# Optimization experiments

Hardware: AMD Instinct MI355X
Metric: run time of the kernel (lower is better)

Reference implementation:

```python
import jax, jax.numpy as jnp
import numpy as np

T, B, D, H = 512, 64, 1024, 1024


def setup_inputs() -> dict:
    key = jax.random.key(0)
    ks = jax.random.split(key, 6)
    s_in = 0.02  # small init so tanh/sigmoid don't saturate
    return {
        "x": jax.random.normal(ks[0], (T, B, D), jnp.float32),
        "Wih": jax.random.normal(ks[1], (D, 4 * H), jnp.float32) * s_in,
        "Whh": jax.random.normal(ks[2], (H, 4 * H), jnp.float32) * s_in,
        "b": jnp.zeros((4 * H,), jnp.float32),
        "Wih_r": jax.random.normal(ks[3], (D, 4 * H), jnp.float32) * s_in,
        "Whh_r": jax.random.normal(ks[4], (H, 4 * H), jnp.float32) * s_in,
        "b_r": jnp.zeros((4 * H,), jnp.float32),
    }


def _lstm_scan(x, Wih, Whh, b):
    """Run an LSTM over time-major x [T,B,D]; returns (hs [T,B,H], h_T, c_T)."""
    Bsz = x.shape[1]
    h0 = jnp.zeros((Bsz, H), x.dtype)
    c0 = jnp.zeros((Bsz, H), x.dtype)

    # Precompute input projections for all timesteps in one big GEMM.
    xg = jnp.einsum("tbd,dg->tbg", x, Wih) + b  # [T,B,4H]

    def step(carry, xg_t):
        h, c = carry
        gates = xg_t + h @ Whh  # [B,4H]
        i, f, g, o = jnp.split(gates, 4, axis=-1)
        c_next = jax.nn.sigmoid(f) * c + jax.nn.sigmoid(i) * jnp.tanh(g)
        h_next = jax.nn.sigmoid(o) * jnp.tanh(c_next)
        return (h_next, c_next), h_next

    (hT, cT), hs = jax.lax.scan(step, (h0, c0), xg)
    return hs, hT, cT


def reference(x, Wih, Whh, b, Wih_r, Whh_r, b_r):
    # forward direction
    hs_f, hT, cT = _lstm_scan(x, Wih, Whh, b)
    # backward direction: flip time, run, flip outputs back
    hs_b, _, _ = _lstm_scan(x[::-1], Wih_r, Whh_r, b_r)
    output = jnp.concatenate([hs_f, hs_b[::-1]], axis=-1)  # [T,B,2H]
    # original returns (output, h_n) where h_n is the forward cell's final (h, c)
    return output, hT, cT
```

## Files before the change

### kernel.cpp

```cpp
#include <hip/hip_runtime.h>
#include <hip/hip_bf16.h>


#define TS    512
#define BATCH 64
#define DDIM  1024
#define HDIM  1024
#define KD    2048
#define GD    4096
#define OUT_HS ((size_t)TS * BATCH * 2 * HDIM)
#define HT_OFF OUT_HS
#define CT_OFF (OUT_HS + (size_t)BATCH * HDIM)

#define WP_BYTES   ((size_t)2 * GD * KD * 2)
#define XBF_BYTES  ((size_t)TS * BATCH * DDIM * 2)
#define HS_BYTES   ((size_t)2 * 2 * BATCH * HDIM * 2)
#define BAR_BYTES  ((size_t)4096)
#define WS_A_TOTAL (WP_BYTES + XBF_BYTES + HS_BYTES + BAR_BYTES)
#define WS_B_TOTAL (WP_BYTES + HS_BYTES + BAR_BYTES)

typedef __attribute__((ext_vector_type(8))) short frag8;
typedef __attribute__((ext_vector_type(4))) float f32x4;
typedef unsigned long long u64;

__device__ __forceinline__ ushort f2b(float f) {
  union { float f; unsigned u; } v; v.f = f;
  unsigned r = v.u + 0x7FFFu + ((v.u >> 16) & 1u);
  return (ushort)(r >> 16);
}
__device__ __forceinline__ float sigf(float x) { return 1.0f / (1.0f + __expf(-x)); }
__device__ __forceinline__ float tanh_fast(float x) {
  x = fminf(15.0f, fmaxf(-15.0f, x));
  float e = __expf(2.0f * x);
  return (e - 1.0f) / (e + 1.0f);
}


__global__ void xconv(const float* __restrict__ x, ushort* __restrict__ o) {
  size_t i = ((size_t)blockIdx.x * 256 + threadIdx.x) * 8;
  float4 a = *(const float4*)(x + i);
  float4 b = *(const float4*)(x + i + 4);
  union { ushort s[8]; uint4 v; } r;
  r.s[0] = f2b(a.x); r.s[1] = f2b(a.y); r.s[2] = f2b(a.z); r.s[3] = f2b(a.w);
  r.s[4] = f2b(b.x); r.s[5] = f2b(b.y); r.s[6] = f2b(b.z); r.s[7] = f2b(b.w);
  *(uint4*)(o + i) = r.v;
}

__global__ void wpackk(const float* __restrict__ Wih,  const float* __restrict__ Whh,
                       const float* __restrict__ WihR, const float* __restrict__ WhhR,
                       ushort* __restrict__ wp) {
  __shared__ ushort tile[32][36];
  int bid = blockIdx.x;
  int kt  = bid & 63;
  int pt  = (bid >> 6) & 127;
  int dir = bid >> 13;
  const float* Wi = dir ? WihR : Wih;
  const float* Wh = dir ? WhhR : Whh;
  int t  = threadIdx.x;
  int kl = t >> 3;
  int g  = (t >> 1) & 3;
  int q  = t & 1;
  int k  = kt * 32 + kl;
  const float* srow = (k < 1024) ? (Wi + (size_t)k * GD) : (Wh + (size_t)(k - 1024) * GD);
  float4 v = *(const float4*)(srow + g * 1024 + pt * 8 + q * 4);
  int pl = g * 8 + q * 4;
  tile[kl][pl + 0] = f2b(v.x); tile[kl][pl + 1] = f2b(v.y);
  tile[kl][pl + 2] = f2b(v.z); tile[kl][pl + 3] = f2b(v.w);
  __syncthreads();
  int po = t >> 3;
  int kc = t & 7;
  ushort* dst = wp + ((size_t)dir * GD + pt * 32 + po) * KD + kt * 32 + kc * 4;
  ushort4 ov;
  ov.x = tile[kc * 4 + 0][po]; ov.y = tile[kc * 4 + 1][po];
  ov.z = tile[kc * 4 + 2][po]; ov.w = tile[kc * 4 + 3][po];
  *(ushort4*)dst = ov;
}

#define MFMA(a, b, c) __builtin_amdgcn_mfma_f32_16x16x32_bf16((a), (b), (c), 0, 0, 0)
#define ALOADU64(p) __hip_atomic_load((p), __ATOMIC_RELAXED, __HIP_MEMORY_SCOPE_AGENT)
#define SB() __builtin_amdgcn_sched_barrier(0)

template <int MODEA>
__global__ __launch_bounds__(256, 1)
void lstm_scan(const ushort* __restrict__ xbf, const float* __restrict__ xf,
               const ushort* __restrict__ wpack,
               const float* __restrict__ bfwd, const float* __restrict__ bbwd,
               ushort* hstate, float* __restrict__ out, unsigned* bar) {
  __shared__ ushort wlds[32 * KD];

  const int tid  = threadIdx.x;
  const int lane = tid & 63;
  const int wv   = tid >> 6;
  const int wg   = blockIdx.x;
  const int dir  = wg >> 7;
  const int wq   = wg & 127;
  unsigned* grpflags = bar + (dir * 4 + wv) * 128;

  {
    const ushort* src = wpack + ((size_t)dir * GD + wq * 32) * KD;
#pragma unroll
    for (int it = 0; it < 32; ++it) {
      int m  = it * 256 + tid;
      int p  = m >> 8;
      int kc = m & 255;
      uint4 v = *(const uint4*)(src + (size_t)p * KD + kc * 8);
      int off = p * 4096 + ((kc * 16) ^ ((p & 7) << 4));
      *(uint4*)((char*)wlds + off) = v;
    }
  }
  __syncthreads();

  const int lm   = lane & 15;
  const int jj   = lane & 7;
  const int kb   = (lane >> 4) * 8;
  const int kb2  = kb * 2;
  const int arow = wv * 16 + lm;
  const int hcol = wq * 8 + jj;
  const int sw   = jj << 4;
  const int b0base = lm * 4096;
  const int b1base = (16 + lm) * 4096;

  const float* bsrc = dir ? bbwd : bfwd;
  const float bias0 = bsrc[(lm >> 3) * HDIM + hcol];
  const float bias1 = bsrc[(2 + (lm >> 3)) * HDIM + hcol];

  float creg[4] = {0.f, 0.f, 0.f, 0.f};
  float hvv[4];
  f32x4 a0a, a0b, a1a, a1b;

  auto compute_x = [&](int tt) {
    const int tsrc = dir ? (TS - 1 - tt) : tt;
    a0a = (f32x4){0.f,0.f,0.f,0.f}; a0b = (f32x4){0.f,0.f,0.f,0.f};
    a1a = (f32x4){0.f,0.f,0.f,0.f}; a1b = (f32x4){0.f,0.f,0.f,0.f};
    if (MODEA) {
      const ushort* xs = xbf + ((size_t)tsrc * BATCH + arow) * DDIM + kb;
#pragma unroll 8
      for (int kk = 0; kk < 32; kk += 2) {
        frag8 a  = *(const frag8*)(xs + kk * 32);
        frag8 a2 = *(const frag8*)(xs + (kk + 1) * 32);
        int ko  = (kk * 64 + kb2) ^ sw;
        int ko2 = ((kk + 1) * 64 + kb2) ^ sw;
        frag8 b0  = *(const frag8*)((const char*)wlds + (b0base + ko));
        frag8 b1  = *(const frag8*)((const char*)wlds + (b1base + ko));
        frag8 b02 = *(const frag8*)((const char*)wlds + (b0base + ko2));
        frag8 b12 = *(const frag8*)((const char*)wlds + (b1base + ko2));
        a0a = MFMA(a, b0, a0a);  a1a = MFMA(a, b1, a1a);
        a0b = MFMA(a2, b02, a0b); a1b = MFMA(a2, b12, a1b);
      }
    } else {
      const float* xs = xf + ((size_t)tsrc * BATCH + arow) * DDIM + kb;
#pragma unroll 4
      for (int kk = 0; kk < 32; ++kk) {
        float4 f0 = *(const float4*)(xs + kk * 32);
        float4 f1 = *(const float4*)(xs + kk * 32 + 4);
        union { ushort s[8]; frag8 fr; } ua;
        ua.s[0] = f2b(f0.x); ua.s[1] = f2b(f0.y); ua.s[2] = f2b(f0.z); ua.s[3] = f2b(f0.w);
        ua.s[4] = f2b(f1.x); ua.s[5] = f2b(f1.y); ua.s[6] = f2b(f1.z); ua.s[7] = f2b(f1.w);
        int ko = (kk * 64 + kb2) ^ sw;
        frag8 b0 = *(const frag8*)((const char*)wlds + (b0base + ko));
        frag8 b1 = *(const frag8*)((const char*)wlds + (b1base + ko));
        if (kk & 1) { a0b = MFMA(ua.fr, b0, a0b); a1b = MFMA(ua.fr, b1, a1b); }
        else        { a0a = MFMA(ua.fr, b0, a0a); a1a = MFMA(ua.fr, b1, a1a); }
      }
    }
  };

  auto h_part = [&](int t) {
    const ushort* hsrd = hstate + (((size_t)(t & 1) * 2 + dir) * BATCH + arow) * HDIM + kb;
    frag8 hf[32];
#pragma unroll
    for (int kk = 0; kk < 32; ++kk)
      asm volatile("global_load_dwordx4 %0, %1, off offset:%2 sc1"
                   : "=v"(hf[kk]) : "v"(hsrd), "i"(kk * 64) : "memory");
    asm volatile("s_waitcnt vmcnt(0)" ::: "memory");
    SB();
#pragma unroll
    for (int kk = 0; kk < 32; kk += 2) {
      int ko  = (2048 + kk * 64 + kb2) ^ sw;
      int ko2 = (2048 + (kk + 1) * 64 + kb2) ^ sw;
      frag8 b0  = *(const frag8*)((const char*)wlds + (b0base + ko));
      frag8 b1  = *(const frag8*)((const char*)wlds + (b1base + ko));
      frag8 b02 = *(const frag8*)((const char*)wlds + (b0base + ko2));
      frag8 b12 = *(const frag8*)((const char*)wlds + (b1base + ko2));
      a0a = MFMA(hf[kk], b0, a0a);      a1a = MFMA(hf[kk], b1, a1a);
      a0b = MFMA(hf[kk + 1], b02, a0b); a1b = MFMA(hf[kk + 1], b12, a1b);
    }
  };

  compute_x(0);

  for (int t = 0; t < TS; ++t) {
    if (t > 0) h_part(t);

    const int tsrc = dir ? (TS - 1 - t) : t;
    f32x4 acc0 = a0a + a0b;
    f32x4 acc1 = a1a + a1b;

    ushort* hnext = hstate + ((size_t)(((t + 1) & 1) * 2 + dir) * BATCH) * HDIM;
    const size_t obase = ((size_t)tsrc * BATCH) * (2 * HDIM) + (size_t)dir * HDIM + hcol;
    const bool last = (t == TS - 1);
    const bool last_f = (dir == 0) && last;

#pragma unroll
    for (int i = 0; i < 4; ++i) {
      float g0 = acc0[i] + bias0;
      float g1 = acc1[i] + bias1;
      float q0 = __shfl_xor(g0, 8);
      float q1 = __shfl_xor(g1, 8);
      if ((lane & 8) == 0) {
        float cn = sigf(q0) * creg[i] + sigf(g0) * tanh_fast(g1);
        creg[i] = cn;
        hvv[i] = sigf(q1) * tanh_fast(cn);
      }
    }

    if (!last) {
#pragma unroll
      for (int i = 0; i < 4; ++i) {
        if ((lane & 8) == 0) {
          int brow = wv * 16 + (lane >> 4) * 4 + i;
          __hip_atomic_store(hnext + (size_t)brow * HDIM + hcol, f2b(hvv[i]),
                             __ATOMIC_RELAXED, __HIP_MEMORY_SCOPE_AGENT);
        }
      }
    }
    SB();
#pragma unroll
    for (int i = 0; i < 4; ++i) {
      if ((lane & 8) == 0) {
        int brow = wv * 16 + (lane >> 4) * 4 + i;
        __builtin_nontemporal_store(hvv[i], out + obase + (size_t)brow * (2 * HDIM));
      }
    }
    if (last_f) {
#pragma unroll
      for (int i = 0; i < 4; ++i) {
        if ((lane & 8) == 0) {
          int brow = wv * 16 + (lane >> 4) * 4 + i;
          __builtin_nontemporal_store(hvv[i], out + HT_OFF + (size_t)brow * HDIM + hcol);
          __builtin_nontemporal_store(creg[i], out + CT_OFF + (size_t)brow * HDIM + hcol);
        }
      }
    }

    if (last) break;

    asm volatile("s_waitcnt vmcnt(4)" ::: "memory");
    if (lane == 0)
      __hip_atomic_store(grpflags + wq, (unsigned)(t + 1),
                         __ATOMIC_RELAXED, __HIP_MEMORY_SCOPE_AGENT);

    compute_x(t + 1);

    {
      const unsigned want = (unsigned)(t + 1);
      const u64* f2 = (const u64*)grpflags + lane;
      for (;;) {
        u64 v = ALOADU64(f2);
        if ((unsigned)v >= want && (unsigned)(v >> 32) >= want) break;
        __builtin_amdgcn_s_sleep(1);
      }
    }
    __atomic_signal_fence(__ATOMIC_SEQ_CST);
    asm volatile("" ::: "memory");
  }
}

extern "C" void kernel_launch(void* const* d_in, const int* in_sizes, int n_in,
                              void* d_out, int out_size, void* d_ws, size_t ws_size,
                              hipStream_t stream) {
  const float* x    = (const float*)d_in[0];
  const float* Wih  = (const float*)d_in[1];
  const float* Whh  = (const float*)d_in[2];
  const float* b    = (const float*)d_in[3];
  const float* WihR = (const float*)d_in[4];
  const float* WhhR = (const float*)d_in[5];
  const float* bR   = (const float*)d_in[6];
  float* out = (float*)d_out;
  char* ws = (char*)d_ws;

  if (ws_size < WS_B_TOTAL) return;
  const bool modeA = (ws_size >= WS_A_TOTAL);

  ushort* wp  = (ushort*)(ws);
  ushort* xbf = (ushort*)(ws + WP_BYTES);
  size_t hs_off = modeA ? (WP_BYTES + XBF_BYTES) : WP_BYTES;
  ushort* hs = (ushort*)(ws + hs_off);
  unsigned* bar = (unsigned*)(ws + hs_off + HS_BYTES);

  hipMemsetAsync(ws + hs_off + HS_BYTES, 0, BAR_BYTES, stream);

  wpackk<<<dim3(16384), dim3(256), 0, stream>>>(Wih, Whh, WihR, WhhR, wp);

  if (modeA) {
    xconv<<<dim3(16384), dim3(256), 0, stream>>>(x, xbf);
    lstm_scan<1><<<dim3(256), dim3(256), 0, stream>>>(xbf, x, wp, b, bR, hs, out, bar);
  } else {
    lstm_scan<0><<<dim3(256), dim3(256), 0, stream>>>(nullptr, x, wp, b, bR, hs, out, bar);
  }
}
```

Before: 4.379 ms.

## Split K across waves with register-resident weights and LDS partial-sum reduction

In the bf16-x path, each wave now owns a quarter of the K dimension for all 64 batch rows. It keeps its slice of the input and recurrent weights in registers instead of re-reading them from LDS every step. Partial accumulators are exchanged through LDS using per-wave flags and reduced before the gate math. The h-state buffer goes from double to triple buffering, and each wave's grid-wide poll now waits on flags published by all wave groups. The goal is to remove repeated LDS weight traffic and spread the h dependency across waves. The cost is extra LDS round-trips, more register pressure, and an intra-block spin on every step.

Result: slower. 5.516 ms (+26.0%).

```diff
diff --git a/kernel.cpp b/kernel.cpp
--- a/kernel.cpp
+++ b/kernel.cpp
@@ -14,7 +14,7 @@
 
 #define WP_BYTES   ((size_t)2 * GD * KD * 2)
 #define XBF_BYTES  ((size_t)TS * BATCH * DDIM * 2)
-#define HS_BYTES   ((size_t)2 * 2 * BATCH * HDIM * 2)
+#define HS_BYTES   ((size_t)3 * 2 * BATCH * HDIM * 2)
 #define BAR_BYTES  ((size_t)4096)
 #define WS_A_TOTAL (WP_BYTES + XBF_BYTES + HS_BYTES + BAR_BYTES)
 #define WS_B_TOTAL (WP_BYTES + HS_BYTES + BAR_BYTES)
@@ -87,6 +87,7 @@
                const float* __restrict__ bfwd, const float* __restrict__ bbwd,
                ushort* hstate, float* __restrict__ out, unsigned* bar) {
   __shared__ ushort wlds[32 * KD];
+  __shared__ unsigned pflag[64];
 
   const int tid  = threadIdx.x;
   const int lane = tid & 63;
@@ -94,7 +95,7 @@
   const int wg   = blockIdx.x;
   const int dir  = wg >> 7;
   const int wq   = wg & 127;
-  unsigned* grpflags = bar + (dir * 4 + wv) * 128;
+  unsigned* pubflag = bar + (dir * 4 + wv) * 128 + wq;
 
   {
     const ushort* src = wpack + ((size_t)dir * GD + wq * 32) * KD;
@@ -108,13 +109,13 @@
       *(uint4*)((char*)wlds + off) = v;
     }
   }
+  if (tid < 64) pflag[tid] = 0;
   __syncthreads();
 
   const int lm   = lane & 15;
   const int jj   = lane & 7;
-  const int kb   = (lane >> 4) * 8;
-  const int kb2  = kb * 2;
-  const int arow = wv * 16 + lm;
+  const int kg   = lane >> 4;
+  const int kb2  = kg * 16;
   const int hcol = wq * 8 + jj;
   const int sw   = jj << 4;
   const int b0base = lm * 4096;
@@ -126,28 +127,185 @@
 
   float creg[4] = {0.f, 0.f, 0.f, 0.f};
   float hvv[4];
-  f32x4 a0a, a0b, a1a, a1b;
-
-  auto compute_x = [&](int tt) {
-    const int tsrc = dir ? (TS - 1 - tt) : tt;
-    a0a = (f32x4){0.f,0.f,0.f,0.f}; a0b = (f32x4){0.f,0.f,0.f,0.f};
-    a1a = (f32x4){0.f,0.f,0.f,0.f}; a1b = (f32x4){0.f,0.f,0.f,0.f};
-    if (MODEA) {
-      const ushort* xs = xbf + ((size_t)tsrc * BATCH + arow) * DDIM + kb;
-#pragma unroll 8
-      for (int kk = 0; kk < 32; kk += 2) {
-        frag8 a  = *(const frag8*)(xs + kk * 32);
-        frag8 a2 = *(const frag8*)(xs + (kk + 1) * 32);
-        int ko  = (kk * 64 + kb2) ^ sw;
-        int ko2 = ((kk + 1) * 64 + kb2) ^ sw;
-        frag8 b0  = *(const frag8*)((const char*)wlds + (b0base + ko));
-        frag8 b1  = *(const frag8*)((const char*)wlds + (b1base + ko));
-        frag8 b02 = *(const frag8*)((const char*)wlds + (b0base + ko2));
-        frag8 b12 = *(const frag8*)((const char*)wlds + (b1base + ko2));
-        a0a = MFMA(a, b0, a0a);  a1a = MFMA(a, b1, a1a);
-        a0b = MFMA(a2, b02, a0b); a1b = MFMA(a2, b12, a1b);
-      }
-    } else {
+
+  if (MODEA) {
+    frag8 Bx0[8], Bx1[8], Bh0[8], Bh1[8];
+#pragma unroll
+    for (int ks = 0; ks < 8; ++ks) {
+      int k0 = (((wv * 8 + ks) * 64 + kb2) ^ sw);
+      int k1 = ((2048 + (wv * 8 + ks) * 64 + kb2) ^ sw);
+      Bx0[ks] = *(const frag8*)((const char*)wlds + b0base + k0);
+      Bx1[ks] = *(const frag8*)((const char*)wlds + b1base + k0);
+      Bh0[ks] = *(const frag8*)((const char*)wlds + b0base + k1);
+      Bh1[ks] = *(const frag8*)((const char*)wlds + b1base + k1);
+    }
+    __syncthreads();
+    f32x4* pb = (f32x4*)wlds;
+
+    f32x4 pacc0[4], pacc1[4];
+
+    auto compute_x = [&](int tt) {
+      const int tsrc = dir ? (TS - 1 - tt) : tt;
+      const ushort* xs = xbf + (size_t)tsrc * BATCH * DDIM + wv * 256 + kg * 8;
+#pragma unroll
+      for (int rt = 0; rt < 4; ++rt) {
+        pacc0[rt] = (f32x4){0.f,0.f,0.f,0.f};
+        pacc1[rt] = (f32x4){0.f,0.f,0.f,0.f};
+      }
+#pragma unroll
+      for (int rt = 0; rt < 4; ++rt) {
+        const ushort* p = xs + (size_t)(rt * 16 + lm) * DDIM;
+        frag8 f[8];
+#pragma unroll
+        for (int ks = 0; ks < 8; ++ks) f[ks] = *(const frag8*)(p + ks * 32);
+#pragma unroll
+        for (int ks = 0; ks < 8; ++ks) {
+          pacc0[rt] = MFMA(f[ks], Bx0[ks], pacc0[rt]);
+          pacc1[rt] = MFMA(f[ks], Bx1[ks], pacc1[rt]);
+        }
+      }
+    };
+
+    auto h_part = [&](int t) {
+      const ushort* hb = hstate + (((size_t)(t % 3) * 2 + dir) * BATCH + lm) * HDIM
+                         + wv * 256 + kg * 8;
+      frag8 hf[32];
+#pragma unroll
+      for (int rt = 0; rt < 4; ++rt) {
+        const ushort* pr = hb + (size_t)(rt * 16) * HDIM;
+#pragma unroll
+        for (int ks = 0; ks < 8; ++ks)
+          asm volatile("global_load_dwordx4 %0, %1, off offset:%2 sc1"
+                       : "=v"(hf[rt * 8 + ks]) : "v"(pr), "i"(ks * 64) : "memory");
+      }
+      asm volatile("s_waitcnt vmcnt(0)" ::: "memory");
+      SB();
+#pragma unroll
+      for (int rt = 0; rt < 4; ++rt)
+#pragma unroll
+        for (int ks = 0; ks < 8; ++ks) {
+          pacc0[rt] = MFMA(hf[rt * 8 + ks], Bh0[ks], pacc0[rt]);
+          pacc1[rt] = MFMA(hf[rt * 8 + ks], Bh1[ks], pacc1[rt]);
+        }
+    };
+
+    auto gpoll = [&](int gen) {
+      const unsigned want = (unsigned)gen;
+      const int wvp = lane >> 4;
+      const u64* f2 = (const u64*)(bar + (dir * 4 + wvp) * 128 + wv * 32) + (lane & 15);
+      for (;;) {
+        u64 v = ALOADU64(f2);
+        if ((unsigned)v >= want && (unsigned)(v >> 32) >= want) break;
+        __builtin_amdgcn_s_sleep(1);
+      }
+      __atomic_signal_fence(__ATOMIC_SEQ_CST);
+      asm volatile("" ::: "memory");
+    };
+
+    compute_x(0);
+
+    for (int t = 0; t < TS; ++t) {
+      if (t > 0) h_part(t);
+
+      const int par = t & 1;
+      {
+        int wbase = ((par * 4 + wv) * 4) * 2 * 64;
+#pragma unroll
+        for (int rt = 0; rt < 4; ++rt) {
+          pb[wbase + (rt * 2 + 0) * 64 + lane] = pacc0[rt];
+          pb[wbase + (rt * 2 + 1) * 64 + lane] = pacc1[rt];
+        }
+        asm volatile("s_waitcnt lgkmcnt(0)" ::: "memory");
+        SB();
+        if (lane == 0)
+          __hip_atomic_store(&pflag[wv * 16], (unsigned)(t + 1),
+                             __ATOMIC_RELAXED, __HIP_MEMORY_SCOPE_WORKGROUP);
+        for (;;) {
+          unsigned m0 = __hip_atomic_load(&pflag[0],  __ATOMIC_RELAXED, __HIP_MEMORY_SCOPE_WORKGROUP);
+          unsigned m1 = __hip_atomic_load(&pflag[16], __ATOMIC_RELAXED, __HIP_MEMORY_SCOPE_WORKGROUP);
+          unsigned m2 = __hip_atomic_load(&pflag[32], __ATOMIC_RELAXED, __HIP_MEMORY_SCOPE_WORKGROUP);
+          unsigned m3 = __hip_atomic_load(&pflag[48], __ATOMIC_RELAXED, __HIP_MEMORY_SCOPE_WORKGROUP);
+          if (m0 > (unsigned)t && m1 > (unsigned)t && m2 > (unsigned)t && m3 > (unsigned)t) break;
+          __builtin_amdgcn_s_sleep(1);
+        }
+        SB();
+        asm volatile("" ::: "memory");
+      }
+      f32x4 acc0 = (f32x4){0.f,0.f,0.f,0.f};
+      f32x4 acc1 = (f32x4){0.f,0.f,0.f,0.f};
+#pragma unroll
+      for (int w = 0; w < 4; ++w) {
+        int rbase = ((par * 4 + w) * 4 + wv) * 2 * 64;
+        acc0 += pb[rbase + 0 * 64 + lane];
+        acc1 += pb[rbase + 1 * 64 + lane];
+      }
+
+      const int tsrc = dir ? (TS - 1 - t) : t;
+      ushort* hnext = hstate + ((size_t)(((t + 1) % 3) * 2 + dir) * BATCH) * HDIM;
+      const size_t obase = ((size_t)tsrc * BATCH) * (2 * HDIM) + (size_t)dir * HDIM + hcol;
+      const bool last = (t == TS - 1);
+      const bool last_f = (dir == 0) && last;
+
+#pragma unroll
+      for (int i = 0; i < 4; ++i) {
+        float g0 = acc0[i] + bias0;
+        float g1 = acc1[i] + bias1;
+        float q0 = __shfl_xor(g0, 8);
+        float q1 = __shfl_xor(g1, 8);
+        if ((lane & 8) == 0) {
+          float cn = sigf(q0) * creg[i] + sigf(g0) * tanh_fast(g1);
+          creg[i] = cn;
+          hvv[i] = sigf(q1) * tanh_fast(cn);
+        }
+      }
+      if (!last) {
+#pragma unroll
+        for (int i = 0; i < 4; ++i) {
+          if ((lane & 8) == 0) {
+            int brow = wv * 16 + (lane >> 4) * 4 + i;
+            __hip_atomic_store(hnext + (size_t)brow * HDIM + hcol, f2b(hvv[i]),
+                               __ATOMIC_RELAXED, __HIP_MEMORY_SCOPE_AGENT);
+          }
+        }
+      }
+      SB();
+#pragma unroll
+      for (int i = 0; i < 4; ++i) {
+        if ((lane & 8) == 0) {
+          int brow = wv * 16 + (lane >> 4) * 4 + i;
+          __builtin_nontemporal_store(hvv[i], out + obase + (size_t)brow * (2 * HDIM));
+        }
+      }
+      if (last_f) {
+#pragma unroll
+        for (int i = 0; i < 4; ++i) {
+          if ((lane & 8) == 0) {
+            int brow = wv * 16 + (lane >> 4) * 4 + i;
+            __builtin_nontemporal_store(hvv[i], out + HT_OFF + (size_t)brow * HDIM + hcol);
+            __builtin_nontemporal_store(creg[i], out + CT_OFF + (size_t)brow * HDIM + hcol);
+          }
+        }
+      }
+
+      if (last) break;
+
+      asm volatile("s_waitcnt vmcnt(4)" ::: "memory");
+      if (lane == 0)
+        __hip_atomic_store(pubflag, (unsigned)(t + 1),
+                           __ATOMIC_RELAXED, __HIP_MEMORY_SCOPE_AGENT);
+
+      compute_x(t + 1);
+      gpoll(t + 1);
+    }
+  } else {
+    const int kb = kg * 8;
+    const int arow = wv * 16 + lm;
+    unsigned* grpflags = bar + (dir * 4 + wv) * 128;
+    f32x4 a0a, a0b, a1a, a1b;
+    auto compute_x_old = [&](int tt) {
+      const int tsrc = dir ? (TS - 1 - tt) : tt;
+      a0a = (f32x4){0.f,0.f,0.f,0.f}; a0b = (f32x4){0.f,0.f,0.f,0.f};
+      a1a = (f32x4){0.f,0.f,0.f,0.f}; a1b = (f32x4){0.f,0.f,0.f,0.f};
       const float* xs = xf + ((size_t)tsrc * BATCH + arow) * DDIM + kb;
 #pragma unroll 4
       for (int kk = 0; kk < 32; ++kk) {
@@ -156,113 +314,82 @@
         union { ushort s[8]; frag8 fr; } ua;
         ua.s[0] = f2b(f0.x); ua.s[1] = f2b(f0.y); ua.s[2] = f2b(f0.z); ua.s[3] = f2b(f0.w);
         ua.s[4] = f2b(f1.x); ua.s[5] = f2b(f1.y); ua.s[6] = f2b(f1.z); ua.s[7] = f2b(f1.w);
-        int ko = (kk * 64 + kb2) ^ sw;
+        int ko = (kk * 64 + kb * 2) ^ sw;
         frag8 b0 = *(const frag8*)((const char*)wlds + (b0base + ko));
         frag8 b1 = *(const frag8*)((const char*)wlds + (b1base + ko));
         if (kk & 1) { a0b = MFMA(ua.fr, b0, a0b); a1b = MFMA(ua.fr, b1, a1b); }
         else        { a0a = MFMA(ua.fr, b0, a0a); a1a = MFMA(ua.fr, b1, a1a); }
       }
+    };
+    auto h_part_old = [&](int t) {
+      const ushort* hsrd = hstate + (((size_t)(t % 3) * 2 + dir) * BATCH + arow) * HDIM + kb;
+      frag8 hf[32];
+#pragma unroll
+      for (int kk = 0; kk < 32; ++kk)
+        asm volatile("global_load_dwordx4 %0, %1, off offset:%2 sc1"
+                     : "=v"(hf[kk]) : "v"(hsrd), "i"(kk * 64) : "memory");
+      asm volatile("s_waitcnt vmcnt(0)" ::: "memory");
+      SB();
+#pragma unroll
+      for (int kk = 0; kk < 32; kk += 2) {
+        int ko  = (2048 + kk * 64 + kb * 2) ^ sw;
+        int ko2 = (2048 + (kk + 1) * 64 + kb * 2) ^ sw;
+        frag8 b0  = *(const frag8*)((const char*)wlds + (b0base + ko));
+        frag8 b1  = *(const frag8*)((const char*)wlds + (b1base + ko));
+        frag8 b02 = *(const frag8*)((const char*)wlds + (b0base + ko2));
+        frag8 b12 = *(const frag8*)((const char*)wlds + (b1base + ko2));
+        a0a = MFMA(hf[kk], b0, a0a);      a1a = MFMA(hf[kk], b1, a1a);
+        a0b = MFMA(hf[kk + 1], b02, a0b); a1b = MFMA(hf[kk + 1], b12, a1b);
+      }
+    };
+    compute_x_old(0);
+    for (int t = 0; t < TS; ++t) {
+      if (t > 0) h_part_old(t);
+      const int tsrc = dir ? (TS - 1 - t) : t;
+      f32x4 acc0 = a0a + a0b, acc1 = a1a + a1b;
+      ushort* hnext = hstate + ((size_t)(((t + 1) % 3) * 2 + dir) * BATCH) * HDIM;
+      const size_t obase = ((size_t)tsrc * BATCH) * (2 * HDIM) + (size_t)dir * HDIM + hcol;
+      const bool last = (t == TS - 1);
+      const bool last_f = (dir == 0) && last;
+#pragma unroll
+      for (int i = 0; i < 4; ++i) {
+        float g0 = acc0[i] + bias0;
+        float g1 = acc1[i] + bias1;
+        float q0 = __shfl_xor(g0, 8);
+        float q1 = __shfl_xor(g1, 8);
+        if ((lane & 8) == 0) {
+          float cn = sigf(q0) * creg[i] + sigf(g0) * tanh_fast(g1);
+          creg[i] = cn;
+          float hv = sigf(q1) * tanh_fast(cn);
+          int brow = wv * 16 + (lane >> 4) * 4 + i;
+          out[obase + (size_t)brow * (2 * HDIM)] = hv;
+          if (!last)
+            __hip_atomic_store(hnext + (size_t)brow * HDIM + hcol, f2b(hv),
+                               __ATOMIC_RELAXED, __HIP_MEMORY_SCOPE_AGENT);
+          if (last_f) {
+            out[HT_OFF + (size_t)brow * HDIM + hcol] = hv;
+            out[CT_OFF + (size_t)brow * HDIM + hcol] = cn;
+          }
+        }
+      }
+      if (last) break;
+      asm volatile("s_waitcnt vmcnt(0)" ::: "memory");
+      if (lane == 0)
+        __hip_atomic_store(grpflags + wq, (unsigned)(t + 1),
+                           __ATOMIC_RELAXED, __HIP_MEMORY_SCOPE_AGENT);
+      compute_x_old(t + 1);
+      {
+        const unsigned want = (unsigned)(t + 1);
+        const u64* f2 = (const u64*)grpflags + lane;
+        for (;;) {
+          u64 v = ALOADU64(f2);
+          if ((unsigned)v >= want && (unsigned)(v >> 32) >= want) break;
+          __builtin_amdgcn_s_sleep(1);
+        }
+      }
+      __atomic_signal_fence(__ATOMIC_SEQ_CST);
+      asm volatile("" ::: "memory");
     }
-  };
-
-  auto h_part = [&](int t) {
-    const ushort* hsrd = hstate + (((size_t)(t & 1) * 2 + dir) * BATCH + arow) * HDIM + kb;
-    frag8 hf[32];
-#pragma unroll
-    for (int kk = 0; kk < 32; ++kk)
-      asm volatile("global_load_dwordx4 %0, %1, off offset:%2 sc1"
-                   : "=v"(hf[kk]) : "v"(hsrd), "i"(kk * 64) : "memory");
-    asm volatile("s_waitcnt vmcnt(0)" ::: "memory");
-    SB();
-#pragma unroll
-    for (int kk = 0; kk < 32; kk += 2) {
-      int ko  = (2048 + kk * 64 + kb2) ^ sw;
-      int ko2 = (2048 + (kk + 1) * 64 + kb2) ^ sw;
-      frag8 b0  = *(const frag8*)((const char*)wlds + (b0base + ko));
-      frag8 b1  = *(const frag8*)((const char*)wlds + (b1base + ko));
-      frag8 b02 = *(const frag8*)((const char*)wlds + (b0base + ko2));
-      frag8 b12 = *(const frag8*)((const char*)wlds + (b1base + ko2));
-      a0a = MFMA(hf[kk], b0, a0a);      a1a = MFMA(hf[kk], b1, a1a);
-      a0b = MFMA(hf[kk + 1], b02, a0b); a1b = MFMA(hf[kk + 1], b12, a1b);
-    }
-  };
-
-  compute_x(0);
-
-  for (int t = 0; t < TS; ++t) {
-    if (t > 0) h_part(t);
-
-    const int tsrc = dir ? (TS - 1 - t) : t;
-    f32x4 acc0 = a0a + a0b;
-    f32x4 acc1 = a1a + a1b;
-
-    ushort* hnext = hstate + ((size_t)(((t + 1) & 1) * 2 + dir) * BATCH) * HDIM;
-    const size_t obase = ((size_t)tsrc * BATCH) * (2 * HDIM) + (size_t)dir * HDIM + hcol;
-    const bool last = (t == TS - 1);
-    const bool last_f = (dir == 0) && last;
-
-#pragma unroll
-    for (int i = 0; i < 4; ++i) {
-      float g0 = acc0[i] + bias0;
-      float g1 = acc1[i] + bias1;
-      float q0 = __shfl_xor(g0, 8);
-      float q1 = __shfl_xor(g1, 8);
-      if ((lane & 8) == 0) {
-        float cn = sigf(q0) * creg[i] + sigf(g0) * tanh_fast(g1);
-        creg[i] = cn;
-        hvv[i] = sigf(q1) * tanh_fast(cn);
-      }
-    }
-
-    if (!last) {
-#pragma unroll
-      for (int i = 0; i < 4; ++i) {
-        if ((lane & 8) == 0) {
-          int brow = wv * 16 + (lane >> 4) * 4 + i;
-          __hip_atomic_store(hnext + (size_t)brow * HDIM + hcol, f2b(hvv[i]),
-                             __ATOMIC_RELAXED, __HIP_MEMORY_SCOPE_AGENT);
-        }
-      }
-    }
-    SB();
-#pragma unroll
-    for (int i = 0; i < 4; ++i) {
-      if ((lane & 8) == 0) {
-        int brow = wv * 16 + (lane >> 4) * 4 + i;
-        __builtin_nontemporal_store(hvv[i], out + obase + (size_t)brow * (2 * HDIM));
-      }
-    }
-    if (last_f) {
-#pragma unroll
-      for (int i = 0; i < 4; ++i) {
-        if ((lane & 8) == 0) {
-          int brow = wv * 16 + (lane >> 4) * 4 + i;
-          __builtin_nontemporal_store(hvv[i], out + HT_OFF + (size_t)brow * HDIM + hcol);
-          __builtin_nontemporal_store(creg[i], out + CT_OFF + (size_t)brow * HDIM + hcol);
-        }
-      }
-    }
-
-    if (last) break;
-
-    asm volatile("s_waitcnt vmcnt(4)" ::: "memory");
-    if (lane == 0)
-      __hip_atomic_store(grpflags + wq, (unsigned)(t + 1),
-                         __ATOMIC_RELAXED, __HIP_MEMORY_SCOPE_AGENT);
-
-    compute_x(t + 1);
-
-    {
-      const unsigned want = (unsigned)(t + 1);
-      const u64* f2 = (const u64*)grpflags + lane;
-      for (;;) {
-        u64 v = ALOADU64(f2);
-        if ((unsigned)v >= want && (unsigned)(v >> 32) >= want) break;
-        __builtin_amdgcn_s_sleep(1);
-      }
-    }
-    __atomic_signal_fence(__ATOMIC_SEQ_CST);
-    asm volatile("" ::: "memory");
   }
 }
 
```

## Split K dimension across two wave groups per block with LDS partial-sum reduction

Applied to the files above, without the earlier changes.

Doubles the block to 512 threads so that each of the four row waves gets a partner wave handling the other half of the K dimension for both the x and h projections. The partner writes its partial accumulators to shared memory and signals through a workgroup-scope LDS flag, and the primary wave adds them before computing the gates. This halves the serial per-wave MFMA and h-load chain on the recurrent critical path. In exchange it adds an intra-block handoff and more waves contending for LDS bandwidth. The fallback mode keeps the old single-wave path and lets the extra waves exit early.

Measured after the change: 4.916 ms. 1.12x slower.

```diff
diff --git a/kernel.cpp b/kernel.cpp
--- a/kernel.cpp
+++ b/kernel.cpp
@@ -81,16 +81,20 @@
 #define SB() __builtin_amdgcn_sched_barrier(0)
 
 template <int MODEA>
-__global__ __launch_bounds__(256, 1)
+__global__ __launch_bounds__(512, 1)
 void lstm_scan(const ushort* __restrict__ xbf, const float* __restrict__ xf,
                const ushort* __restrict__ wpack,
                const float* __restrict__ bfwd, const float* __restrict__ bbwd,
                ushort* hstate, float* __restrict__ out, unsigned* bar) {
   __shared__ ushort wlds[32 * KD];
+  __shared__ f32x4 pbuf[2][4][2][64];
+  __shared__ unsigned hflag[2][4][16];
 
   const int tid  = threadIdx.x;
   const int lane = tid & 63;
-  const int wv   = tid >> 6;
+  const int w8   = tid >> 6;
+  const int wv   = w8 & 3;
+  const int khalf= w8 >> 2;
   const int wg   = blockIdx.x;
   const int dir  = wg >> 7;
   const int wq   = wg & 127;
@@ -99,8 +103,8 @@
   {
     const ushort* src = wpack + ((size_t)dir * GD + wq * 32) * KD;
 #pragma unroll
-    for (int it = 0; it < 32; ++it) {
-      int m  = it * 256 + tid;
+    for (int it = 0; it < 16; ++it) {
+      int m  = it * 512 + tid;
       int p  = m >> 8;
       int kc = m & 255;
       uint4 v = *(const uint4*)(src + (size_t)p * KD + kc * 8);
@@ -108,17 +112,20 @@
       *(uint4*)((char*)wlds + off) = v;
     }
   }
+  if (tid < 128) ((unsigned*)hflag)[tid] = 0;
   __syncthreads();
 
   const int lm   = lane & 15;
   const int jj   = lane & 7;
-  const int kb   = (lane >> 4) * 8;
+  const int kg   = lane >> 4;
+  const int kb   = kg * 8;
   const int kb2  = kb * 2;
   const int arow = wv * 16 + lm;
   const int hcol = wq * 8 + jj;
   const int sw   = jj << 4;
   const int b0base = lm * 4096;
   const int b1base = (16 + lm) * 4096;
+  const int ksb  = khalf * 16;
 
   const float* bsrc = dir ? bbwd : bfwd;
   const float bias0 = bsrc[(lm >> 3) * HDIM + hcol];
@@ -128,18 +135,30 @@
   float hvv[4];
   f32x4 a0a, a0b, a1a, a1b;
 
-  auto compute_x = [&](int tt) {
-    const int tsrc = dir ? (TS - 1 - tt) : tt;
-    a0a = (f32x4){0.f,0.f,0.f,0.f}; a0b = (f32x4){0.f,0.f,0.f,0.f};
-    a1a = (f32x4){0.f,0.f,0.f,0.f}; a1b = (f32x4){0.f,0.f,0.f,0.f};
-    if (MODEA) {
-      const ushort* xs = xbf + ((size_t)tsrc * BATCH + arow) * DDIM + kb;
+  auto poll = [&](int gen) {
+    const unsigned want = (unsigned)gen;
+    const u64* f2 = (const u64*)grpflags + lane;
+    for (;;) {
+      u64 v = ALOADU64(f2);
+      if ((unsigned)v >= want && (unsigned)(v >> 32) >= want) break;
+      __builtin_amdgcn_s_sleep(1);
+    }
+    __atomic_signal_fence(__ATOMIC_SEQ_CST);
+    asm volatile("" ::: "memory");
+  };
+
+  if (MODEA) {
+    auto compute_x = [&](int tt) {
+      const int tsrc = dir ? (TS - 1 - tt) : tt;
+      a0a = (f32x4){0.f,0.f,0.f,0.f}; a0b = (f32x4){0.f,0.f,0.f,0.f};
+      a1a = (f32x4){0.f,0.f,0.f,0.f}; a1b = (f32x4){0.f,0.f,0.f,0.f};
+      const ushort* xs = xbf + ((size_t)tsrc * BATCH + arow) * DDIM + ksb * 32 + kb;
 #pragma unroll 8
-      for (int kk = 0; kk < 32; kk += 2) {
+      for (int kk = 0; kk < 16; kk += 2) {
         frag8 a  = *(const frag8*)(xs + kk * 32);
         frag8 a2 = *(const frag8*)(xs + (kk + 1) * 32);
-        int ko  = (kk * 64 + kb2) ^ sw;
-        int ko2 = ((kk + 1) * 64 + kb2) ^ sw;
+        int ko  = (((ksb + kk) * 64) + kb2) ^ sw;
+        int ko2 = (((ksb + kk + 1) * 64) + kb2) ^ sw;
         frag8 b0  = *(const frag8*)((const char*)wlds + (b0base + ko));
         frag8 b1  = *(const frag8*)((const char*)wlds + (b1base + ko));
         frag8 b02 = *(const frag8*)((const char*)wlds + (b0base + ko2));
@@ -147,7 +166,121 @@
         a0a = MFMA(a, b0, a0a);  a1a = MFMA(a, b1, a1a);
         a0b = MFMA(a2, b02, a0b); a1b = MFMA(a2, b12, a1b);
       }
-    } else {
+    };
+
+    auto h_part = [&](int t) {
+      const ushort* hsrd = hstate + (((size_t)(t & 1) * 2 + dir) * BATCH + arow) * HDIM
+                           + ksb * 32 + kb;
+      frag8 hf[16];
+#pragma unroll
+      for (int kk = 0; kk < 16; ++kk)
+        asm volatile("global_load_dwordx4 %0, %1, off offset:%2 sc1"
+                     : "=v"(hf[kk]) : "v"(hsrd), "i"(kk * 64) : "memory");
+      asm volatile("s_waitcnt vmcnt(0)" ::: "memory");
+      SB();
+#pragma unroll
+      for (int kk = 0; kk < 16; kk += 2) {
+        int ko  = (2048 + (ksb + kk) * 64 + kb2) ^ sw;
+        int ko2 = (2048 + (ksb + kk + 1) * 64 + kb2) ^ sw;
+        frag8 b0  = *(const frag8*)((const char*)wlds + (b0base + ko));
+        frag8 b1  = *(const frag8*)((const char*)wlds + (b1base + ko));
+        frag8 b02 = *(const frag8*)((const char*)wlds + (b0base + ko2));
+        frag8 b12 = *(const frag8*)((const char*)wlds + (b1base + ko2));
+        a0a = MFMA(hf[kk], b0, a0a);      a1a = MFMA(hf[kk], b1, a1a);
+        a0b = MFMA(hf[kk + 1], b02, a0b); a1b = MFMA(hf[kk + 1], b12, a1b);
+      }
+    };
+
+    compute_x(0);
+
+    for (int t = 0; t < TS; ++t) {
+      if (t > 0) h_part(t);
+      const int par = t & 1;
+      const bool last = (t == TS - 1);
+
+      if (khalf == 1) {
+        pbuf[par][wv][0][lane] = a0a + a0b;
+        pbuf[par][wv][1][lane] = a1a + a1b;
+        asm volatile("s_waitcnt lgkmcnt(0)" ::: "memory");
+        SB();
+        if (lane == 0)
+          __hip_atomic_store(&hflag[par][wv][0], (unsigned)(t + 1),
+                             __ATOMIC_RELAXED, __HIP_MEMORY_SCOPE_WORKGROUP);
+        if (last) break;
+        compute_x(t + 1);
+        poll(t + 1);
+      } else {
+        f32x4 acc0 = a0a + a0b;
+        f32x4 acc1 = a1a + a1b;
+        while (__hip_atomic_load(&hflag[par][wv][0], __ATOMIC_RELAXED,
+                                 __HIP_MEMORY_SCOPE_WORKGROUP) < (unsigned)(t + 1))
+          __builtin_amdgcn_s_sleep(1);
+        SB();
+        asm volatile("" ::: "memory");
+        acc0 += pbuf[par][wv][0][lane];
+        acc1 += pbuf[par][wv][1][lane];
+
+        const int tsrc = dir ? (TS - 1 - t) : t;
+        ushort* hnext = hstate + ((size_t)(((t + 1) & 1) * 2 + dir) * BATCH) * HDIM;
+        const size_t obase = ((size_t)tsrc * BATCH) * (2 * HDIM) + (size_t)dir * HDIM + hcol;
+        const bool last_f = (dir == 0) && last;
+
+#pragma unroll
+        for (int i = 0; i < 4; ++i) {
+          float g0 = acc0[i] + bias0;
+          float g1 = acc1[i] + bias1;
+          float q0 = __shfl_xor(g0, 8);
+          float q1 = __shfl_xor(g1, 8);
+          if ((lane & 8) == 0) {
+            float cn = sigf(q0) * creg[i] + sigf(g0) * tanh_fast(g1);
+            creg[i] = cn;
+            hvv[i] = sigf(q1) * tanh_fast(cn);
+          }
+        }
+        if (!last) {
+#pragma unroll
+          for (int i = 0; i < 4; ++i) {
+            if ((lane & 8) == 0) {
+              int brow = wv * 16 + (lane >> 4) * 4 + i;
+              __hip_atomic_store(hnext + (size_t)brow * HDIM + hcol, f2b(hvv[i]),
+                                 __ATOMIC_RELAXED, __HIP_MEMORY_SCOPE_AGENT);
+            }
+          }
+        }
+        SB();
+#pragma unroll
+        for (int i = 0; i < 4; ++i) {
+          if ((lane & 8) == 0) {
+            int brow = wv * 16 + (lane >> 4) * 4 + i;
+            __builtin_nontemporal_store(hvv[i], out + obase + (size_t)brow * (2 * HDIM));
+          }
+        }
+        if (last_f) {
+#pragma unroll
+          for (int i = 0; i < 4; ++i) {
+            if ((lane & 8) == 0) {
+              int brow = wv * 16 + (lane >> 4) * 4 + i;
+              __builtin_nontemporal_store(hvv[i], out + HT_OFF + (size_t)brow * HDIM + hcol);
+              __builtin_nontemporal_store(creg[i], out + CT_OFF + (size_t)brow * HDIM + hcol);
+            }
+          }
+        }
+        if (last) break;
+
+        asm volatile("s_waitcnt vmcnt(4)" ::: "memory");
+        if (lane == 0)
+          __hip_atomic_store(grpflags + wq, (unsigned)(t + 1),
+                             __ATOMIC_RELAXED, __HIP_MEMORY_SCOPE_AGENT);
+        compute_x(t + 1);
+        poll(t + 1);
+      }
+    }
+  } else {
+    if (khalf == 1) return;
+    auto compute_x_old = [&](int tt) {
+      const int tsrc = dir ? (TS - 1 - tt) : tt;
+      a0a = (f32x4){0.f,0.f,0.f,0.f}; a0b = (f32x4){0.f,0.f,0.f,0.f};
+      a1a = (f32x4){0.f,0.f,0.f,0.f}; a1b = (f32x4){0.f,0.f,0.f,0.f};
       const float* xs = xf + ((size_t)tsrc * BATCH + arow) * DDIM + kb;
 #pragma unroll 4
       for (int kk = 0; kk < 32; ++kk) {
@@ -162,107 +295,66 @@
         if (kk & 1) { a0b = MFMA(ua.fr, b0, a0b); a1b = MFMA(ua.fr, b1, a1b); }
         else        { a0a = MFMA(ua.fr, b0, a0a); a1a = MFMA(ua.fr, b1, a1a); }
       }
+    };
+    auto h_part_old = [&](int t) {
+      const ushort* hsrd = hstate + (((size_t)(t & 1) * 2 + dir) * BATCH + arow) * HDIM + kb;
+      frag8 hf[32];
+#pragma unroll
+      for (int kk = 0; kk < 32; ++kk)
+        asm volatile("global_load_dwordx4 %0, %1, off offset:%2 sc1"
+                     : "=v"(hf[kk]) : "v"(hsrd), "i"(kk * 64) : "memory");
+      asm volatile("s_waitcnt vmcnt(0)" ::: "memory");
+      SB();
+#pragma unroll
+      for (int kk = 0; kk < 32; kk += 2) {
+        int ko  = (2048 + kk * 64 + kb2) ^ sw;
+        int ko2 = (2048 + (kk + 1) * 64 + kb2) ^ sw;
+        frag8 b0  = *(const frag8*)((const char*)wlds + (b0base + ko));
+        frag8 b1  = *(const frag8*)((const char*)wlds + (b1base + ko));
+        frag8 b02 = *(const frag8*)((const char*)wlds + (b0base + ko2));
+        frag8 b12 = *(const frag8*)((const char*)wlds + (b1base + ko2));
+        a0a = MFMA(hf[kk], b0, a0a);      a1a = MFMA(hf[kk], b1, a1a);
+        a0b = MFMA(hf[kk + 1], b02, a0b); a1b = MFMA(hf[kk + 1], b12, a1b);
+      }
+    };
+    compute_x_old(0);
+    for (int t = 0; t < TS; ++t) {
+      if (t > 0) h_part_old(t);
+      const int tsrc = dir ? (TS - 1 - t) : t;
+      f32x4 acc0 = a0a + a0b, acc1 = a1a + a1b;
+      ushort* hnext = hstate + ((size_t)(((t + 1) & 1) * 2 + dir) * BATCH) * HDIM;
+      const size_t obase = ((size_t)tsrc * BATCH) * (2 * HDIM) + (size_t)dir * HDIM + hcol;
+      const bool last = (t == TS - 1);
+      const bool last_f = (dir == 0) && last;
+#pragma unroll
+      for (int i = 0; i < 4; ++i) {
+        float g0 = acc0[i] + bias0;
+        float g1 = acc1[i] + bias1;
+        float q0 = __shfl_xor(g0, 8);
+        float q1 = __shfl_xor(g1, 8);
+        if ((lane & 8) == 0) {
+          float cn = sigf(q0) * creg[i] + sigf(g0) * tanh_fast(g1);
+          creg[i] = cn;
+          float hv = sigf(q1) * tanh_fast(cn);
+          int brow = wv * 16 + (lane >> 4) * 4 + i;
+          out[obase + (size_t)brow * (2 * HDIM)] = hv;
+          if (!last)
+            __hip_atomic_store(hnext + (size_t)brow * HDIM + hcol, f2b(hv),
+                               __ATOMIC_RELAXED, __HIP_MEMORY_SCOPE_AGENT);
+          if (last_f) {
+            out[HT_OFF + (size_t)brow * HDIM + hcol] = hv;
+            out[CT_OFF + (size_t)brow * HDIM + hcol] = cn;
+          }
+        }
+      }
+      if (last) break;
+      asm volatile("s_waitcnt vmcnt(0)" ::: "memory");
+      if (lane == 0)
+        __hip_atomic_store(grpflags + wq, (unsigned)(t + 1),
+                           __ATOMIC_RELAXED, __HIP_MEMORY_SCOPE_AGENT);
+      compute_x_old(t + 1);
+      poll(t + 1);
     }
-  };
-
-  auto h_part = [&](int t) {
-    const ushort* hsrd = hstate + (((size_t)(t & 1) * 2 + dir) * BATCH + arow) * HDIM + kb;
-    frag8 hf[32];
-#pragma unroll
-    for (int kk = 0; kk < 32; ++kk)
-      asm volatile("global_load_dwordx4 %0, %1, off offset:%2 sc1"
-                   : "=v"(hf[kk]) : "v"(hsrd), "i"(kk * 64) : "memory");
-    asm volatile("s_waitcnt vmcnt(0)" ::: "memory");
-    SB();
-#pragma unroll
-    for (int kk = 0; kk < 32; kk += 2) {
-      int ko  = (2048 + kk * 64 + kb2) ^ sw;
-      int ko2 = (2048 + (kk + 1) * 64 + kb2) ^ sw;
-      frag8 b0  = *(const frag8*)((const char*)wlds + (b0base + ko));
-      frag8 b1  = *(const frag8*)((const char*)wlds + (b1base + ko));
-      frag8 b02 = *(const frag8*)((const char*)wlds + (b0base + ko2));
-      frag8 b12 = *(const frag8*)((const char*)wlds + (b1base + ko2));
-      a0a = MFMA(hf[kk], b0, a0a);      a1a = MFMA(hf[kk], b1, a1a);
-      a0b = MFMA(hf[kk + 1], b02, a0b); a1b = MFMA(hf[kk + 1], b12, a1b);
-    }
-  };
-
-  compute_x(0);
-
-  for (int t = 0; t < TS; ++t) {
-    if (t > 0) h_part(t);
-
-    const int tsrc = dir ? (TS - 1 - t) : t;
-    f32x4 acc0 = a0a + a0b;
-    f32x4 acc1 = a1a + a1b;
-
-    ushort* hnext = hstate + ((size_t)(((t + 1) & 1) * 2 + dir) * BATCH) * HDIM;
-    const size_t obase = ((size_t)tsrc * BATCH) * (2 * HDIM) + (size_t)dir * HDIM + hcol;
-    const bool last = (t == TS - 1);
-    const bool last_f = (dir == 0) && last;
-
-#pragma unroll
-    for (int i = 0; i < 4; ++i) {
-      float g0 = acc0[i] + bias0;
-      float g1 = acc1[i] + bias1;
-      float q0 = __shfl_xor(g0, 8);
-      float q1 = __shfl_xor(g1, 8);
-      if ((lane & 8) == 0) {
-        float cn = sigf(q0) * creg[i] + sigf(g0) * tanh_fast(g1);
-        creg[i] = cn;
-        hvv[i] = sigf(q1) * tanh_fast(cn);
-      }
-    }
-
-    if (!last) {
-#pragma unroll
-      for (int i = 0; i < 4; ++i) {
-        if ((lane & 8) == 0) {
-          int brow = wv * 16 + (lane >> 4) * 4 + i;
-          __hip_atomic_store(hnext + (size_t)brow * HDIM + hcol, f2b(hvv[i]),
-                             __ATOMIC_RELAXED, __HIP_MEMORY_SCOPE_AGENT);
-        }
-      }
-    }
-    SB();
-#pragma unroll
-    for (int i = 0; i < 4; ++i) {
-      if ((lane & 8) == 0) {
-        int brow = wv * 16 + (lane >> 4) * 4 + i;
-        __builtin_nontemporal_store(hvv[i], out + obase + (size_t)brow * (2 * HDIM));
-      }
-    }
-    if (last_f) {
-#pragma unroll
-      for (int i = 0; i < 4; ++i) {
-        if ((lane & 8) == 0) {
-          int brow = wv * 16 + (lane >> 4) * 4 + i;
-          __builtin_nontemporal_store(hvv[i], out + HT_OFF + (size_t)brow * HDIM + hcol);
-          __builtin_nontemporal_store(creg[i], out + CT_OFF + (size_t)brow * HDIM + hcol);
-        }
-      }
-    }
-
-    if (last) break;
-
-    asm volatile("s_waitcnt vmcnt(4)" ::: "memory");
-    if (lane == 0)
-      __hip_atomic_store(grpflags + wq, (unsigned)(t + 1),
-                         __ATOMIC_RELAXED, __HIP_MEMORY_SCOPE_AGENT);
-
-    compute_x(t + 1);
-
-    {
-      const unsigned want = (unsigned)(t + 1);
-      const u64* f2 = (const u64*)grpflags + lane;
-      for (;;) {
-        u64 v = ALOADU64(f2);
-        if ((unsigned)v >= want && (unsigned)(v >> 32) >= want) break;
-        __builtin_amdgcn_s_sleep(1);
-      }
-    }
-    __atomic_signal_fence(__ATOMIC_SEQ_CST);
-    asm volatile("" ::: "memory");
   }
 }
 
@@ -294,8 +386,8 @@
 
   if (modeA) {
     xconv<<<dim3(16384), dim3(256), 0, stream>>>(x, xbf);
-    lstm_scan<1><<<dim3(256), dim3(256), 0, stream>>>(xbf, x, wp, b, bR, hs, out, bar);
+    lstm_scan<1><<<dim3(256), dim3(512), 0, stream>>>(xbf, x, wp, b, bR, hs, out, bar);
   } else {
-    lstm_scan<0><<<dim3(256), dim3(256), 0, stream>>>(nullptr, x, wp, b, bR, hs, out, bar);
+    lstm_scan<0><<<dim3(256), dim3(512), 0, stream>>>(nullptr, x, wp, b, bR, hs, out, bar);
   }
 }
```
